# Kernel optimization log

Hardware: AMD Instinct MI355X
Metric: run time of the kernel (lower is better)

## Reference

```python
import jax, jax.numpy as jnp
import numpy as np

DIM = 1024
NUM_HEADS = 16
HEAD_DIM = DIM // NUM_HEADS
SCALE = HEAD_DIM ** -0.5


def setup_inputs() -> dict:
    key = jax.random.key(0)
    k1, k2, k3, k4 = jax.random.split(key, 4)
    x = jax.random.normal(k1, (4, 2048, DIM), dtype=jnp.float32)
    # torch nn.Linear(dim, 3*dim, bias=False): weight shape [3*dim, dim]
    w_qkv = jax.random.normal(k2, (3 * DIM, DIM), dtype=jnp.float32) * (DIM ** -0.5)
    # torch nn.Linear(dim, dim): weight [dim, dim], bias [dim]
    w_proj = jax.random.normal(k3, (DIM, DIM), dtype=jnp.float32) * (DIM ** -0.5)
    b_proj = jax.random.normal(k4, (DIM,), dtype=jnp.float32) * 0.01
    return {"x": x, "w_qkv": w_qkv, "w_proj": w_proj, "b_proj": b_proj}


def reference(x, w_qkv, w_proj, b_proj):
    B, N, C = x.shape
    # qkv: [B, N, 3*C] -> [3, B, H, N, Dh]
    qkv = (x @ w_qkv.T).reshape(B, N, 3, NUM_HEADS, HEAD_DIM)
    qkv = jnp.transpose(qkv, (2, 0, 3, 1, 4))
    q, k, v = qkv[0], qkv[1], qkv[2]
    # full score matrix, as in the original module
    attn = jnp.einsum("bhqd,bhkd->bhqk", q, k) * SCALE
    attn = jax.nn.softmax(attn, axis=-1)
    out = jnp.einsum("bhqk,bhkd->bhqd", attn, v)  # [B,H,N,Dh]
    out = jnp.transpose(out, (0, 2, 1, 3)).reshape(B, N, C)
    return out @ w_proj.T + b_proj
```

## Files before the change

kernel.cpp:

```cpp
#include <hip/hip_runtime.h>
#include <stdint.h>

#define DIM 1024
#define SEQ 2048
#define BATCH 4
#define ROWS (BATCH*SEQ)
#define QSCALE 0.1803368801111f

typedef __attribute__((ext_vector_type(8))) short bf16x8;
typedef __attribute__((ext_vector_type(4))) float f32x4;
typedef __attribute__((ext_vector_type(8))) _Float16 f16x8;
typedef __attribute__((ext_vector_type(2))) __fp16 fp16x2_raw;

#if __has_builtin(__builtin_amdgcn_exp2f)
#define EXP2F(x) __builtin_amdgcn_exp2f(x)
#else
#define EXP2F(x) __expf((x) * 0.69314718056f)
#endif

#define MFMA_BF16_K32(a,b,c) __builtin_amdgcn_mfma_f32_16x16x32_bf16(a,b,c,0,0,0)
#define MFMA_F16_K32(a,b,c)  __builtin_amdgcn_mfma_f32_16x16x32_f16(a,b,c,0,0,0)

__device__ __forceinline__ unsigned short f2bf(float f) {
  union { float f; unsigned int u; } v; v.f = f;
  unsigned int u = v.u;
  return (unsigned short)((u + 0x7FFFu + ((u >> 16) & 1u)) >> 16);
}

__device__ __forceinline__ unsigned short f2h(float f) {
  union { _Float16 h; unsigned short u; } v;
  v.h = (_Float16)f;
  return v.u;
}

__device__ __forceinline__ unsigned int pkrtz_bits(float lo, float hi) {
  union { fp16x2_raw h; unsigned int u; } v;
  v.h = __builtin_amdgcn_cvt_pkrtz(lo, hi);
  return v.u;
}

__device__ __forceinline__ void gload_lds16(const void* g, void* l) {
  __builtin_amdgcn_global_load_lds(
      (const __attribute__((address_space(1))) unsigned int*)g,
      (__attribute__((address_space(3))) unsigned int*)l,
      16, 0, 0);
}

__global__ void cast_all(const float* __restrict__ x,
                         const float* __restrict__ wq,
                         const float* __restrict__ wp,
                         unsigned short* __restrict__ xb,
                         unsigned short* __restrict__ wqb,
                         unsigned short* __restrict__ wpb) {
  const int i = (blockIdx.x * blockDim.x + threadIdx.x) * 4;
  const float* src;
  unsigned short* dst;
  int off;
  if (i < ROWS * DIM)                 { src = x;  dst = xb;  off = i; }
  else if (i < ROWS * DIM + 3 * DIM * DIM) { src = wq; dst = wqb; off = i - ROWS * DIM; }
  else                                { src = wp; dst = wpb; off = i - ROWS * DIM - 3 * DIM * DIM; }
  float4 f = *(const float4*)(src + off);
  ushort4 o;
  o.x = f2bf(f.x); o.y = f2bf(f.y); o.z = f2bf(f.z); o.w = f2bf(f.w);
  *(ushort4*)(dst + off) = o;
}

__global__ __launch_bounds__(256) void gemm_qkv(
    const unsigned short* __restrict__ A,
    const unsigned short* __restrict__ W,
    unsigned short* __restrict__ qb,
    unsigned short* __restrict__ kb,
    unsigned short* __restrict__ vtb) {
  const int K = DIM;
  __shared__ unsigned short Al[128 * 32];
  __shared__ unsigned short Wl[128 * 32];
  const int tid  = threadIdx.x;
  const int wave = tid >> 6, lane = tid & 63;
  const int quad = lane >> 4, l16 = lane & 15;
  const int m0 = blockIdx.y * 128, n0 = blockIdx.x * 128;
  const int wr = (wave >> 1) * 64, wc = (wave & 1) * 64;
  const int which = n0 >> 10;

  f32x4 acc[4][4];
#pragma unroll
  for (int i = 0; i < 4; i++)
#pragma unroll
    for (int j = 0; j < 4; j++) acc[i][j] = (f32x4)0.f;

  const int arow = wave * 16 + (lane >> 2);
  const int acol = (lane & 3) * 8;
  const unsigned short* Ag = A + (size_t)(m0 + arow) * K + acol;
  const unsigned short* Wg = W + (size_t)(n0 + arow) * K + acol;

  if (which < 2) {
    for (int kt = 0; kt < K; kt += 32) {
      __syncthreads();
#pragma unroll
      for (int i = 0; i < 2; i++) {
        gload_lds16((const void*)(Ag + (size_t)(i * 64) * K + kt), (void*)&Al[i * 2048 + wave * 512]);
        gload_lds16((const void*)(Wg + (size_t)(i * 64) * K + kt), (void*)&Wl[i * 2048 + wave * 512]);
      }
      __syncthreads();
      bf16x8 af[4], wf[4];
#pragma unroll
      for (int i = 0; i < 4; i++) {
        af[i] = *(const bf16x8*)&Al[(wr + i * 16 + l16) * 32 + quad * 8];
        wf[i] = *(const bf16x8*)&Wl[(wc + i * 16 + l16) * 32 + quad * 8];
      }
#pragma unroll
      for (int i = 0; i < 4; i++)
#pragma unroll
        for (int j = 0; j < 4; j++)
          acc[i][j] = __builtin_amdgcn_mfma_f32_16x16x32_bf16(wf[j], af[i], acc[i][j], 0, 0, 0);
    }
    const float sc = (which == 0) ? QSCALE : 1.f;
    unsigned short* base = (which == 0) ? qb : kb;
#pragma unroll
    for (int i = 0; i < 4; i++) {
      const int tok = m0 + wr + i * 16 + l16;
      const int b = tok >> 11, n = tok & 2047;
#pragma unroll
      for (int j = 0; j < 4; j++) {
        const int col0 = n0 + wc + j * 16 + quad * 4;
        const int h = (col0 >> 6) & 15, d = col0 & 63;
        ushort4 o4;
        o4.x = f2bf(acc[i][j][0] * sc); o4.y = f2bf(acc[i][j][1] * sc);
        o4.z = f2bf(acc[i][j][2] * sc); o4.w = f2bf(acc[i][j][3] * sc);
        *(ushort4*)&base[((size_t)(b * 16 + h) * SEQ + n) * 64 + d] = o4;
      }
    }
  } else {
    for (int kt = 0; kt < K; kt += 32) {
      __syncthreads();
#pragma unroll
      for (int i = 0; i < 2; i++) {
        gload_lds16((const void*)(Ag + (size_t)(i * 64) * K + kt), (void*)&Al[i * 2048 + wave * 512]);
        gload_lds16((const void*)(Wg + (size_t)(i * 64) * K + kt), (void*)&Wl[i * 2048 + wave * 512]);
      }
      __syncthreads();
      bf16x8 af[4], wf[4];
#pragma unroll
      for (int i = 0; i < 4; i++) {
        af[i] = *(const bf16x8*)&Al[(wr + i * 16 + l16) * 32 + quad * 8];
        wf[i] = *(const bf16x8*)&Wl[(wc + i * 16 + l16) * 32 + quad * 8];
      }
#pragma unroll
      for (int i = 0; i < 4; i++)
#pragma unroll
        for (int j = 0; j < 4; j++)
          acc[i][j] = __builtin_amdgcn_mfma_f32_16x16x32_bf16(af[i], wf[j], acc[i][j], 0, 0, 0);
    }
#pragma unroll
    for (int i = 0; i < 4; i++) {
      const int row = m0 + wr + i * 16 + quad * 4;
      const int b = row >> 11, n = row & 2047;
#pragma unroll
      for (int j = 0; j < 4; j++) {
        const int col = n0 + wc + j * 16 + l16;
        const int h = (col >> 6) & 15, d = col & 63;
        ushort4 o4;
        o4.x = f2h(acc[i][j][0]); o4.y = f2h(acc[i][j][1]);
        o4.z = f2h(acc[i][j][2]); o4.w = f2h(acc[i][j][3]);
        *(ushort4*)&vtb[((size_t)(b * 16 + h) * 64 + d) * SEQ + n] = o4;
      }
    }
  }
}

__global__ __launch_bounds__(256, 2) void attn_kernel(
    const unsigned short* __restrict__ qb,
    const unsigned short* __restrict__ kb,
    const unsigned short* __restrict__ vtb,
    unsigned short* __restrict__ out) {
  __shared__ unsigned short Kl[2][64 * 64];
  __shared__ unsigned short Vl[2][64 * 64];

  const int tid  = threadIdx.x;
  const int wave = tid >> 6, lane = tid & 63;
  const int quad = lane >> 4, l16 = lane & 15;
  const int bh    = blockIdx.x;
  const int qtile = blockIdx.y;
  const size_t qkbase = (size_t)bh * SEQ * 64;
  const int q0 = qtile * 256 + wave * 64;

  bf16x8 qf[4][2];
#pragma unroll
  for (int mi = 0; mi < 4; mi++)
#pragma unroll
    for (int kk = 0; kk < 2; kk++)
      qf[mi][kk] = *(const bf16x8*)&qb[qkbase + (size_t)(q0 + mi * 16 + l16) * 64 + kk * 32 + quad * 8];

  f32x4 o[4][4];
#pragma unroll
  for (int mi = 0; mi < 4; mi++)
#pragma unroll
    for (int nt = 0; nt < 4; nt++) o[mi][nt] = (f32x4)0.f;
  f32x4 lacc[4];
#pragma unroll
  for (int mi = 0; mi < 4; mi++) lacc[mi] = (f32x4)0.f;

  union { f16x8 v; unsigned int d[4]; } ones8;
#pragma unroll
  for (int j = 0; j < 4; j++) ones8.d[j] = 0x3C003C00u;

  const unsigned short* Kg = kb + qkbase;
  const unsigned short* Vg = vtb + (size_t)bh * 64 * SEQ;
  const int srow = tid >> 3;
  const int schk = tid & 7;
  const int swK = (srow & 3) | (((srow >> 3) & 1) << 2);
  const int swV = srow & 7;

  auto stage = [&](int kt, int buf) {
#pragma unroll
    for (int p = 0; p < 2; p++) {
      const int r = p * 32 + srow;
      gload_lds16((const void*)(Kg + (size_t)(kt + r) * 64 + (schk ^ swK) * 8),
                  (void*)&Kl[buf][p * 2048 + wave * 512]);
      gload_lds16((const void*)(Vg + (size_t)r * SEQ + kt + (schk ^ swV) * 8),
                  (void*)&Vl[buf][p * 2048 + wave * 512]);
    }
  };

  stage(0, 0);

  const int rbase = ((l16 >> 2) << 3) + (l16 & 3);
  const int sR = (l16 & 3) | (((l16 >> 2) & 1) << 2);

  int buf = 0;
  for (int kt = 0; kt < SEQ; kt += 64, buf ^= 1) {
    __syncthreads();
    if (kt + 64 < SEQ) stage(kt + 64, buf ^ 1);

#pragma unroll
    for (int kk = 0; kk < 2; kk++) {
      bf16x8 kf[2][2];
#pragma unroll
      for (int T = 0; T < 2; T++) {
        const int R = kk * 32 + rbase + 4 * T;
        kf[T][0] = *(const bf16x8*)&Kl[buf][R * 64 + ((quad ^ sR) << 3)];
        kf[T][1] = *(const bf16x8*)&Kl[buf][R * 64 + (((4 + quad) ^ sR) << 3)];
      }
      f16x8 vf[4];
#pragma unroll
      for (int nt = 0; nt < 4; nt++) {
        const int vr = nt * 16 + l16;
        vf[nt] = *(const f16x8*)&Vl[buf][vr * 64 + (((kk * 4 + quad) ^ (vr & 7)) << 3)];
      }
#pragma unroll
      for (int mi = 0; mi < 4; mi++) {
        f32x4 s0 = (f32x4)0.f, s1 = (f32x4)0.f;
        s0 = MFMA_BF16_K32(kf[0][0], qf[mi][0], s0);
        s0 = MFMA_BF16_K32(kf[0][1], qf[mi][1], s0);
        s1 = MFMA_BF16_K32(kf[1][0], qf[mi][0], s1);
        s1 = MFMA_BF16_K32(kf[1][1], qf[mi][1], s1);
        union { f16x8 v; unsigned int d[4]; } pu;
        pu.d[0] = pkrtz_bits(EXP2F(s0[0]), EXP2F(s0[1]));
        pu.d[1] = pkrtz_bits(EXP2F(s0[2]), EXP2F(s0[3]));
        pu.d[2] = pkrtz_bits(EXP2F(s1[0]), EXP2F(s1[1]));
        pu.d[3] = pkrtz_bits(EXP2F(s1[2]), EXP2F(s1[3]));
        lacc[mi] = MFMA_F16_K32(pu.v, ones8.v, lacc[mi]);
#pragma unroll
        for (int nt = 0; nt < 4; nt++)
          o[mi][nt] = MFMA_F16_K32(pu.v, vf[nt], o[mi][nt]);
      }
    }
  }

  const int h = bh & 15, b = bh >> 4;
#pragma unroll
  for (int mi = 0; mi < 4; mi++) {
    float inv[4];
#pragma unroll
    for (int r = 0; r < 4; r++) inv[r] = 1.f / lacc[mi][r];
#pragma unroll
    for (int nt = 0; nt < 4; nt++)
#pragma unroll
      for (int r = 0; r < 4; r++)
        out[((size_t)(b * SEQ + q0 + mi * 16 + quad * 4 + r)) * DIM + h * 64 + nt * 16 + l16] =
            f2bf(o[mi][nt][r] * inv[r]);
  }
}

__global__ __launch_bounds__(256) void gemm_proj(
    const unsigned short* __restrict__ A,
    const unsigned short* __restrict__ W,
    float* __restrict__ out,
    const float* __restrict__ bias) {
  const int N = DIM, K = DIM;
  __shared__ unsigned short Al[128 * 32];
  __shared__ unsigned short Wl[128 * 32];
  const int tid  = threadIdx.x;
  const int wave = tid >> 6, lane = tid & 63;
  const int quad = lane >> 4, l16 = lane & 15;
  const int m0 = blockIdx.y * 128, n0 = blockIdx.x * 128;
  const int wr = (wave >> 1) * 64, wc = (wave & 1) * 64;

  f32x4 acc[4][4];
#pragma unroll
  for (int i = 0; i < 4; i++)
#pragma unroll
    for (int j = 0; j < 4; j++) acc[i][j] = (f32x4)0.f;

  const int arow = wave * 16 + (lane >> 2);
  const int acol = (lane & 3) * 8;
  const unsigned short* Ag = A + (size_t)(m0 + arow) * K + acol;
  const unsigned short* Wg = W + (size_t)(n0 + arow) * K + acol;

  for (int kt = 0; kt < K; kt += 32) {
    __syncthreads();
#pragma unroll
    for (int i = 0; i < 2; i++) {
      gload_lds16((const void*)(Ag + (size_t)(i * 64) * K + kt), (void*)&Al[i * 2048 + wave * 512]);
      gload_lds16((const void*)(Wg + (size_t)(i * 64) * K + kt), (void*)&Wl[i * 2048 + wave * 512]);
    }
    __syncthreads();

    bf16x8 af[4], wf[4];
#pragma unroll
    for (int i = 0; i < 4; i++) {
      af[i] = *(const bf16x8*)&Al[(wr + i * 16 + l16) * 32 + quad * 8];
      wf[i] = *(const bf16x8*)&Wl[(wc + i * 16 + l16) * 32 + quad * 8];
    }
#pragma unroll
    for (int i = 0; i < 4; i++)
#pragma unroll
      for (int j = 0; j < 4; j++)
        acc[i][j] = __builtin_amdgcn_mfma_f32_16x16x32_bf16(af[i], wf[j], acc[i][j], 0, 0, 0);
  }

#pragma unroll
  for (int i = 0; i < 4; i++) {
    const int row = m0 + wr + i * 16 + quad * 4;
#pragma unroll
    for (int j = 0; j < 4; j++) {
      const int col = n0 + wc + j * 16 + l16;
      const float bv = bias[col];
#pragma unroll
      for (int r = 0; r < 4; r++)
        out[(size_t)(row + r) * N + col] = acc[i][j][r] + bv;
    }
  }
}

extern "C" void kernel_launch(void* const* d_in, const int* in_sizes, int n_in,
                              void* d_out, int out_size, void* d_ws, size_t ws_size,
                              hipStream_t stream) {
  const float* x      = (const float*)d_in[0];
  const float* w_qkv  = (const float*)d_in[1];
  const float* w_proj = (const float*)d_in[2];
  const float* b_proj = (const float*)d_in[3];
  float* outp = (float*)d_out;

  char* ws = (char*)d_ws;
  unsigned short* xb     = (unsigned short*)(ws);
  unsigned short* wqkvb  = (unsigned short*)(ws + (16u << 20));
  unsigned short* wprojb = (unsigned short*)(ws + (22u << 20));
  unsigned short* qb     = (unsigned short*)(ws + (24u << 20));
  unsigned short* kb     = (unsigned short*)(ws + (40u << 20));
  unsigned short* vtb    = (unsigned short*)(ws + (56u << 20));
  unsigned short* aout   = (unsigned short*)(ws + (72u << 20));

  const int total4 = (ROWS * DIM + 3 * DIM * DIM + DIM * DIM) / 4;
  cast_all<<<total4 / 256, 256, 0, stream>>>(x, w_qkv, w_proj, xb, wqkvb, wprojb);

  gemm_qkv<<<dim3(24, 64), 256, 0, stream>>>(xb, wqkvb, qb, kb, vtb);
  attn_kernel<<<dim3(64, 8), 256, 0, stream>>>(qb, kb, vtb, aout);
  gemm_proj<<<dim3(8, 64), 256, 0, stream>>>(aout, wprojb, outp, b_proj);
}
```

Before: 257.5 us.

## Swizzle GEMM LDS tiles and triple-buffer attention with 8 waves per block

Applies an XOR swizzle to the LDS layout in both GEMM kernels so fragment reads avoid bank conflicts. The attention kernel moves to 512 threads with 32 queries per wave and a three-stage K/V LDS ring that uses explicit vmcnt waits and raw barriers instead of __syncthreads. It also raises the priority of the MFMA sections with s_setprio. Each wave now holds fewer registers, but the block uses more LDS and sync relies on hand-written waitcnt, which risks a race if the counts are wrong.

```diff
diff --git a/kernel.cpp b/kernel.cpp
--- a/kernel.cpp
+++ b/kernel.cpp
@@ -88,9 +88,10 @@
     for (int j = 0; j < 4; j++) acc[i][j] = (f32x4)0.f;
 
   const int arow = wave * 16 + (lane >> 2);
-  const int acol = (lane & 3) * 8;
+  const int acol = ((lane & 3) ^ ((lane >> 3) & 3)) * 8;
   const unsigned short* Ag = A + (size_t)(m0 + arow) * K + acol;
   const unsigned short* Wg = W + (size_t)(n0 + arow) * K + acol;
+  const int sA = (l16 >> 1) & 3;
 
   if (which < 2) {
     for (int kt = 0; kt < K; kt += 32) {
@@ -104,8 +105,8 @@
       bf16x8 af[4], wf[4];
 #pragma unroll
       for (int i = 0; i < 4; i++) {
-        af[i] = *(const bf16x8*)&Al[(wr + i * 16 + l16) * 32 + quad * 8];
-        wf[i] = *(const bf16x8*)&Wl[(wc + i * 16 + l16) * 32 + quad * 8];
+        af[i] = *(const bf16x8*)&Al[(wr + i * 16 + l16) * 32 + ((quad ^ sA) << 3)];
+        wf[i] = *(const bf16x8*)&Wl[(wc + i * 16 + l16) * 32 + ((quad ^ sA) << 3)];
       }
 #pragma unroll
       for (int i = 0; i < 4; i++)
@@ -141,8 +142,8 @@
       bf16x8 af[4], wf[4];
 #pragma unroll
       for (int i = 0; i < 4; i++) {
-        af[i] = *(const bf16x8*)&Al[(wr + i * 16 + l16) * 32 + quad * 8];
-        wf[i] = *(const bf16x8*)&Wl[(wc + i * 16 + l16) * 32 + quad * 8];
+        af[i] = *(const bf16x8*)&Al[(wr + i * 16 + l16) * 32 + ((quad ^ sA) << 3)];
+        wf[i] = *(const bf16x8*)&Wl[(wc + i * 16 + l16) * 32 + ((quad ^ sA) << 3)];
       }
 #pragma unroll
       for (int i = 0; i < 4; i++)
@@ -167,13 +168,13 @@
   }
 }
 
-__global__ __launch_bounds__(256, 2) void attn_kernel(
+__global__ __launch_bounds__(512, 4) void attn_kernel(
     const unsigned short* __restrict__ qb,
     const unsigned short* __restrict__ kb,
     const unsigned short* __restrict__ vtb,
     unsigned short* __restrict__ out) {
-  __shared__ unsigned short Kl[2][64 * 64];
-  __shared__ unsigned short Vl[2][64 * 64];
+  __shared__ unsigned short Kl[3][64 * 64];
+  __shared__ unsigned short Vl[3][64 * 64];
 
   const int tid  = threadIdx.x;
   const int wave = tid >> 6, lane = tid & 63;
@@ -181,23 +182,23 @@
   const int bh    = blockIdx.x;
   const int qtile = blockIdx.y;
   const size_t qkbase = (size_t)bh * SEQ * 64;
-  const int q0 = qtile * 256 + wave * 64;
-
-  bf16x8 qf[4][2];
-#pragma unroll
-  for (int mi = 0; mi < 4; mi++)
+  const int q0 = qtile * 256 + wave * 32;
+
+  bf16x8 qf[2][2];
+#pragma unroll
+  for (int mi = 0; mi < 2; mi++)
 #pragma unroll
     for (int kk = 0; kk < 2; kk++)
       qf[mi][kk] = *(const bf16x8*)&qb[qkbase + (size_t)(q0 + mi * 16 + l16) * 64 + kk * 32 + quad * 8];
 
-  f32x4 o[4][4];
-#pragma unroll
-  for (int mi = 0; mi < 4; mi++)
+  f32x4 o[2][4];
+#pragma unroll
+  for (int mi = 0; mi < 2; mi++)
 #pragma unroll
     for (int nt = 0; nt < 4; nt++) o[mi][nt] = (f32x4)0.f;
-  f32x4 lacc[4];
-#pragma unroll
-  for (int mi = 0; mi < 4; mi++) lacc[mi] = (f32x4)0.f;
+  f32x4 lacc[2];
+#pragma unroll
+  for (int mi = 0; mi < 2; mi++) lacc[mi] = (f32x4)0.f;
 
   union { f16x8 v; unsigned int d[4]; } ones8;
 #pragma unroll
@@ -210,26 +211,28 @@
   const int swK = (srow & 3) | (((srow >> 3) & 1) << 2);
   const int swV = srow & 7;
 
-  auto stage = [&](int kt, int buf) {
-#pragma unroll
-    for (int p = 0; p < 2; p++) {
-      const int r = p * 32 + srow;
-      gload_lds16((const void*)(Kg + (size_t)(kt + r) * 64 + (schk ^ swK) * 8),
-                  (void*)&Kl[buf][p * 2048 + wave * 512]);
-      gload_lds16((const void*)(Vg + (size_t)r * SEQ + kt + (schk ^ swV) * 8),
-                  (void*)&Vl[buf][p * 2048 + wave * 512]);
-    }
+  auto stage = [&](int kt, int b) {
+    gload_lds16((const void*)(Kg + (size_t)(kt + srow) * 64 + (schk ^ swK) * 8),
+                (void*)&Kl[b][wave * 512]);
+    gload_lds16((const void*)(Vg + (size_t)srow * SEQ + kt + (schk ^ swV) * 8),
+                (void*)&Vl[b][wave * 512]);
   };
 
   stage(0, 0);
+  stage(64, 1);
 
   const int rbase = ((l16 >> 2) << 3) + (l16 & 3);
   const int sR = (l16 & 3) | (((l16 >> 2) & 1) << 2);
 
-  int buf = 0;
-  for (int kt = 0; kt < SEQ; kt += 64, buf ^= 1) {
-    __syncthreads();
-    if (kt + 64 < SEQ) stage(kt + 64, buf ^ 1);
+  int b0 = 0, b1 = 1, b2 = 2;
+  for (int t = 0; t < 32; ++t) {
+    if (t < 31) asm volatile("s_waitcnt vmcnt(2) lgkmcnt(0)" ::: "memory");
+    else        asm volatile("s_waitcnt vmcnt(0) lgkmcnt(0)" ::: "memory");
+    __builtin_amdgcn_s_barrier();
+    if (t + 2 < 32) stage((t + 2) * 64, b2);
+
+    const unsigned short* Kc = &Kl[b0][0];
+    const unsigned short* Vc = &Vl[b0][0];
 
 #pragma unroll
     for (int kk = 0; kk < 2; kk++) {
@@ -237,38 +240,43 @@
 #pragma unroll
       for (int T = 0; T < 2; T++) {
         const int R = kk * 32 + rbase + 4 * T;
-        kf[T][0] = *(const bf16x8*)&Kl[buf][R * 64 + ((quad ^ sR) << 3)];
-        kf[T][1] = *(const bf16x8*)&Kl[buf][R * 64 + (((4 + quad) ^ sR) << 3)];
+        kf[T][0] = *(const bf16x8*)&Kc[R * 64 + ((quad ^ sR) << 3)];
+        kf[T][1] = *(const bf16x8*)&Kc[R * 64 + (((4 + quad) ^ sR) << 3)];
       }
       f16x8 vf[4];
 #pragma unroll
       for (int nt = 0; nt < 4; nt++) {
         const int vr = nt * 16 + l16;
-        vf[nt] = *(const f16x8*)&Vl[buf][vr * 64 + (((kk * 4 + quad) ^ (vr & 7)) << 3)];
-      }
-#pragma unroll
-      for (int mi = 0; mi < 4; mi++) {
+        vf[nt] = *(const f16x8*)&Vc[vr * 64 + (((kk * 4 + quad) ^ (vr & 7)) << 3)];
+      }
+#pragma unroll
+      for (int mi = 0; mi < 2; mi++) {
         f32x4 s0 = (f32x4)0.f, s1 = (f32x4)0.f;
+        __builtin_amdgcn_s_setprio(1);
         s0 = MFMA_BF16_K32(kf[0][0], qf[mi][0], s0);
         s0 = MFMA_BF16_K32(kf[0][1], qf[mi][1], s0);
         s1 = MFMA_BF16_K32(kf[1][0], qf[mi][0], s1);
         s1 = MFMA_BF16_K32(kf[1][1], qf[mi][1], s1);
+        __builtin_amdgcn_s_setprio(0);
         union { f16x8 v; unsigned int d[4]; } pu;
         pu.d[0] = pkrtz_bits(EXP2F(s0[0]), EXP2F(s0[1]));
         pu.d[1] = pkrtz_bits(EXP2F(s0[2]), EXP2F(s0[3]));
         pu.d[2] = pkrtz_bits(EXP2F(s1[0]), EXP2F(s1[1]));
         pu.d[3] = pkrtz_bits(EXP2F(s1[2]), EXP2F(s1[3]));
+        __builtin_amdgcn_s_setprio(1);
         lacc[mi] = MFMA_F16_K32(pu.v, ones8.v, lacc[mi]);
 #pragma unroll
         for (int nt = 0; nt < 4; nt++)
           o[mi][nt] = MFMA_F16_K32(pu.v, vf[nt], o[mi][nt]);
-      }
-    }
+        __builtin_amdgcn_s_setprio(0);
+      }
+    }
+    const int tmp = b0; b0 = b1; b1 = b2; b2 = tmp;
   }
 
   const int h = bh & 15, b = bh >> 4;
 #pragma unroll
-  for (int mi = 0; mi < 4; mi++) {
+  for (int mi = 0; mi < 2; mi++) {
     float inv[4];
 #pragma unroll
     for (int r = 0; r < 4; r++) inv[r] = 1.f / lacc[mi][r];
@@ -302,9 +310,10 @@
     for (int j = 0; j < 4; j++) acc[i][j] = (f32x4)0.f;
 
   const int arow = wave * 16 + (lane >> 2);
-  const int acol = (lane & 3) * 8;
+  const int acol = ((lane & 3) ^ ((lane >> 3) & 3)) * 8;
   const unsigned short* Ag = A + (size_t)(m0 + arow) * K + acol;
   const unsigned short* Wg = W + (size_t)(n0 + arow) * K + acol;
+  const int sA = (l16 >> 1) & 3;
 
   for (int kt = 0; kt < K; kt += 32) {
     __syncthreads();
@@ -318,8 +327,8 @@
     bf16x8 af[4], wf[4];
 #pragma unroll
     for (int i = 0; i < 4; i++) {
-      af[i] = *(const bf16x8*)&Al[(wr + i * 16 + l16) * 32 + quad * 8];
-      wf[i] = *(const bf16x8*)&Wl[(wc + i * 16 + l16) * 32 + quad * 8];
+      af[i] = *(const bf16x8*)&Al[(wr + i * 16 + l16) * 32 + ((quad ^ sA) << 3)];
+      wf[i] = *(const bf16x8*)&Wl[(wc + i * 16 + l16) * 32 + ((quad ^ sA) << 3)];
     }
 #pragma unroll
     for (int i = 0; i < 4; i++)
@@ -364,6 +373,6 @@
   cast_all<<<total4 / 256, 256, 0, stream>>>(x, w_qkv, w_proj, xb, wqkvb, wprojb);
 
   gemm_qkv<<<dim3(24, 64), 256, 0, stream>>>(xb, wqkvb, qb, kb, vtb);
-  attn_kernel<<<dim3(64, 8), 256, 0, stream>>>(qb, kb, vtb, aout);
+  attn_kernel<<<dim3(64, 8), 512, 0, stream>>>(qb, kb, vtb, aout);
   gemm_proj<<<dim3(8, 64), 256, 0, stream>>>(aout, wprojb, outp, b_proj);
 }
```

Measured after the change: 256.6 us. Within noise of the previous version (-0.4%).
